# Kernel optimization log

Hardware: AMD Instinct MI355X
Metric: run time of the kernel (lower is better)

Reference implementation:

```python
import jax, jax.numpy as jnp
import numpy as np

DIM = 128
HEADS = 4
DIM_HEAD = 32
HIDDEN = HEADS * DIM_HEAD  # 128
SCALE = DIM_HEAD ** -0.5


def setup_inputs() -> dict:
    key = jax.random.key(0)
    k1, k2, k3, k4 = jax.random.split(key, 4)
    x = jax.random.normal(k1, (16, DIM, 128, 128), dtype=jnp.float32)
    # 1x1 convs are just channel matmuls: store as [out_ch, in_ch]
    w_qkv = jax.random.normal(k2, (3 * HIDDEN, DIM), dtype=jnp.float32) * (DIM ** -0.5)
    w_out = jax.random.normal(k3, (DIM, HIDDEN), dtype=jnp.float32) * (HIDDEN ** -0.5)
    b_out = jax.random.normal(k4, (DIM,), dtype=jnp.float32) * 0.01
    return {"x": x, "w_qkv": w_qkv, "w_out": w_out, "b_out": b_out}


def reference(x, w_qkv, w_out, b_out):
    b, c, h, w = x.shape
    n = h * w
    # 1x1 conv (no bias): [b, 3*hidden, h, w]
    qkv = jnp.einsum('bchw,oc->bohw', x, w_qkv)
    q, k, v = jnp.split(qkv, 3, axis=1)
    # b (heads d) h w -> b heads d n
    def to_heads(t):
        return t.reshape(b, HEADS, DIM_HEAD, n)
    q = to_heads(q) * SCALE
    k = jax.nn.softmax(to_heads(k), axis=-1)
    v = to_heads(v)
    # small d x e context per (b, head)
    context = jnp.einsum('bhdn,bhen->bhde', k, v)
    out = jnp.einsum('bhde,bhdn->bhen', context, q)  # [b, heads, e, n]
    out = out.reshape(b, HIDDEN, h, w)
    # 1x1 conv with bias
    return jnp.einsum('bchw,oc->bohw', out, w_out) + b_out[None, :, None, None]
```

## Files before the change

kernel.cpp:

```cpp
#include <hip/hip_runtime.h>

typedef float f4 __attribute__((ext_vector_type(4)));
typedef short s4 __attribute__((ext_vector_type(4)));
typedef short s8 __attribute__((ext_vector_type(8)));
typedef unsigned int u32;

#define SCALE 0.17677669529663687f

static __device__ __forceinline__ short bf16c(float f) {
  u32 u = __builtin_bit_cast(u32, f);
  u32 r = u + 0x7fffu + ((u >> 16) & 1u);
  return (short)(r >> 16);
}

static __device__ __forceinline__ f4 mfma32(s8 a, s8 b, f4 c) {
  return __builtin_amdgcn_mfma_f32_16x16x32_bf16(a, b, c, 0, 0, 0);
}
static __device__ __forceinline__ f4 bmm16(s4 a, s4 b, f4 c) {
  s8 A = {a[0], a[1], a[2], a[3], (short)0, (short)0, (short)0, (short)0};
  s8 B = {b[0], b[1], b[2], b[3], (short)0, (short)0, (short)0, (short)0};
  return __builtin_amdgcn_mfma_f32_16x16x32_bf16(A, B, c, 0, 0, 0);
}

#define XSTRIDE 280

__global__ __launch_bounds__(256) void ctx_kernel(
    const float* __restrict__ x, const float* __restrict__ wqkv,
    float* __restrict__ cp, float* __restrict__ zp)
{
  const int chunk = blockIdx.x, b = blockIdx.y;
  const int tid = threadIdx.x, lane = tid & 63, h = tid >> 6;
  __shared__ __align__(16) char lds[2 * 64 * XSTRIDE];

  s8 wf[4][4];
  {
    const int colr = lane & 15, g = lane >> 4;
#pragma unroll
    for (int s = 0; s < 4; ++s) {
      const int grow = (s < 2 ? 128 : 256) + h * 32 + (s & 1) * 16 + colr;
#pragma unroll
      for (int kc = 0; kc < 4; ++kc) {
        const float* src = wqkv + grow * 128 + kc * 32 + g * 8;
        const f4 a = *(const f4*)src;
        const f4 c2 = *(const f4*)(src + 4);
        s8 t = {bf16c(a[0]), bf16c(a[1]), bf16c(a[2]), bf16c(a[3]),
                bf16c(c2[0]), bf16c(c2[1]), bf16c(c2[2]), bf16c(c2[3])};
        wf[s][kc] = t;
      }
    }
  }

  f4 ctxacc[2][2];
#pragma unroll
  for (int a = 0; a < 2; ++a)
#pragma unroll
    for (int e2 = 0; e2 < 2; ++e2) ctxacc[a][e2] = (f4){0.f, 0.f, 0.f, 0.f};
  float zloc[2] = {0.f, 0.f};

  const float* xb = x + (size_t)b * 128 * 16384 + chunk * 1024;
  const int nq = tid & 15, ch = tid >> 4;
  f4 v[2][4];

  auto aload = [&](int tl) {
#pragma unroll
    for (int q = 0; q < 2; ++q) {
      const int c0 = ch * 4 + q * 64;
#pragma unroll
      for (int i = 0; i < 4; ++i)
        v[q][i] = *(const f4*)(xb + (size_t)(c0 + i) * 16384 + tl * 64 + nq * 4);
    }
  };
  auto awrite = [&](int buf) {
#pragma unroll
    for (int q = 0; q < 2; ++q) {
      const int c0 = ch * 4 + q * 64;
#pragma unroll
      for (int j = 0; j < 4; ++j) {
        s4 t = {bf16c(v[q][0][j]), bf16c(v[q][1][j]), bf16c(v[q][2][j]),
                bf16c(v[q][3][j])};
        *(s4*)(lds + buf * (64 * XSTRIDE) + (nq * 4 + j) * XSTRIDE + c0 * 2) = t;
      }
    }
  };
  auto compute = [&](int buf) {
#pragma unroll
    for (int nt = 0; nt < 4; ++nt) {
      const char* rp =
          lds + buf * (64 * XSTRIDE) + (nt * 16 + (lane & 15)) * XSTRIDE +
          (lane >> 4) * 16;
      s8 af[4];
#pragma unroll
      for (int kc = 0; kc < 4; ++kc) {
        const s4 lo = *(const s4*)(rp + kc * 64);
        const s4 hi = *(const s4*)(rp + kc * 64 + 8);
        af[kc] = __builtin_shufflevector(lo, hi, 0, 1, 2, 3, 4, 5, 6, 7);
      }
      f4 acc[4];
#pragma unroll
      for (int s = 0; s < 4; ++s) acc[s] = (f4){0.f, 0.f, 0.f, 0.f};
#pragma unroll
      for (int kc = 0; kc < 4; ++kc)
#pragma unroll
        for (int s = 0; s < 4; ++s)
          acc[s] = mfma32(af[kc], wf[s][kc], acc[s]);
      f4 e0, e1;
#pragma unroll
      for (int r = 0; r < 4; ++r) {
        e0[r] = __expf(acc[0][r]);
        e1[r] = __expf(acc[1][r]);
      }
      zloc[0] += e0[0] + e0[1] + e0[2] + e0[3];
      zloc[1] += e1[0] + e1[1] + e1[2] + e1[3];
      const s4 ea0 = {bf16c(e0[0]), bf16c(e0[1]), bf16c(e0[2]), bf16c(e0[3])};
      const s4 ea1 = {bf16c(e1[0]), bf16c(e1[1]), bf16c(e1[2]), bf16c(e1[3])};
      const s4 vb0 = {bf16c(acc[2][0]), bf16c(acc[2][1]), bf16c(acc[2][2]),
                      bf16c(acc[2][3])};
      const s4 vb1 = {bf16c(acc[3][0]), bf16c(acc[3][1]), bf16c(acc[3][2]),
                      bf16c(acc[3][3])};
      ctxacc[0][0] = bmm16(ea0, vb0, ctxacc[0][0]);
      ctxacc[0][1] = bmm16(ea0, vb1, ctxacc[0][1]);
      ctxacc[1][0] = bmm16(ea1, vb0, ctxacc[1][0]);
      ctxacc[1][1] = bmm16(ea1, vb1, ctxacc[1][1]);
    }
  };

  aload(0);
  awrite(0);
  __syncthreads();
  for (int tl = 0; tl < 16; ++tl) {
    if (tl < 15) aload(tl + 1);
    compute(tl & 1);
    if (tl < 15) awrite((tl + 1) & 1);
    __syncthreads();
  }

  {
    const size_t base = (size_t)((b * 4 + h) * 16 + chunk) * 1024;
    const int g4 = (lane >> 4) * 4, cc = lane & 15;
#pragma unroll
    for (int a = 0; a < 2; ++a)
#pragma unroll
      for (int e2 = 0; e2 < 2; ++e2)
#pragma unroll
        for (int r = 0; r < 4; ++r)
          cp[base + (size_t)(a * 16 + g4 + r) * 32 + e2 * 16 + cc] =
              ctxacc[a][e2][r];
  }
#pragma unroll
  for (int s = 0; s < 2; ++s) {
    float z = zloc[s];
    z += __shfl_xor(z, 16);
    z += __shfl_xor(z, 32);
    if (lane < 16)
      zp[((b * 4 + h) * 16 + chunk) * 32 + s * 16 + lane] = z;
  }
}

__global__ __launch_bounds__(256, 2) void makeP(
    const float* __restrict__ cp, const float* __restrict__ zp,
    const float* __restrict__ wout, const float* __restrict__ wqkv,
    unsigned short* __restrict__ Phi)
{
  const int rg = blockIdx.x, b = blockIdx.y, t = threadIdx.x;
  __shared__ float ctxn[4096];
  __shared__ float zs[128];
  __shared__ float Ms[16][129];

  if (t < 128) {
    float s = 0.f;
#pragma unroll
    for (int ch = 0; ch < 16; ++ch)
      s += zp[((size_t)(b * 4 + (t >> 5)) * 16 + ch) * 32 + (t & 31)];
    zs[t] = s;
  }
  __syncthreads();
  {
    const int i0 = t * 16;
    const int hh = i0 >> 10;
    f4 s0 = {0.f,0.f,0.f,0.f}, s1 = s0, s2 = s0, s3 = s0;
    const float* src = cp + ((size_t)(b * 4 + hh) * 16) * 1024 + (i0 & 1023);
#pragma unroll
    for (int ch = 0; ch < 16; ++ch) {
      const float* p = src + ch * 1024;
      s0 += *(const f4*)(p);
      s1 += *(const f4*)(p + 4);
      s2 += *(const f4*)(p + 8);
      s3 += *(const f4*)(p + 12);
    }
    const float zinv = 1.f / zs[i0 >> 5];
    *(f4*)(ctxn + i0)      = s0 * zinv;
    *(f4*)(ctxn + i0 + 4)  = s1 * zinv;
    *(f4*)(ctxn + i0 + 8)  = s2 * zinv;
    *(f4*)(ctxn + i0 + 12) = s3 * zinv;
  }
  __syncthreads();
  {
    const int o = t >> 4, hd0 = (t & 15) * 8;
    const int hh = hd0 >> 5;
    f4 wseg[8];
    const float* wp = wout + (size_t)(rg * 16 + o) * 128 + hh * 32;
#pragma unroll
    for (int i = 0; i < 8; ++i) wseg[i] = *(const f4*)(wp + i * 4);
#pragma unroll
    for (int j = 0; j < 8; ++j) {
      const float* cn = ctxn + (hd0 + j) * 32;
      f4 acc = {0.f, 0.f, 0.f, 0.f};
#pragma unroll
      for (int i = 0; i < 8; ++i) acc += wseg[i] * *(const f4*)(cn + i * 4);
      Ms[o][hd0 + j] = acc[0] + acc[1] + acc[2] + acc[3];
    }
  }
  __syncthreads();
  {
    const int o = t >> 4, c0 = (t & 15) * 8;
    f4 a0 = {0.f,0.f,0.f,0.f}, a1 = a0;
#pragma unroll 8
    for (int hd = 0; hd < 128; ++hd) {
      const float m = Ms[o][hd];
      const float* wp = wqkv + (size_t)hd * 128 + c0;
      a0 += m * *(const f4*)(wp);
      a1 += m * *(const f4*)(wp + 4);
    }
    a0 *= SCALE;
    a1 *= SCALE;
    s8 out = {bf16c(a0[0]), bf16c(a0[1]), bf16c(a0[2]), bf16c(a0[3]),
              bf16c(a1[0]), bf16c(a1[1]), bf16c(a1[2]), bf16c(a1[3])};
    *(s8*)(Phi + ((size_t)b * 128 + rg * 16 + o) * 128 + c0) = out;
  }
}

__global__ __launch_bounds__(256) void out_gemm(
    const float* __restrict__ x, const unsigned short* __restrict__ Phi,
    const float* __restrict__ bias, float* __restrict__ y)
{
  const int nb = blockIdx.x, b = blockIdx.y;
  const int tid = threadIdx.x, lane = tid & 63, w = tid >> 6;
  __shared__ __align__(16) char lds[128 * XSTRIDE];

  s8 pf[2][4];
#pragma unroll
  for (int ot2 = 0; ot2 < 2; ++ot2) {
    const int orow = (w * 2 + ot2) * 16 + (lane & 15);
#pragma unroll
    for (int kc = 0; kc < 4; ++kc)
      pf[ot2][kc] = *(const s8*)(Phi + ((size_t)b * 128 + orow) * 128 +
                                 kc * 32 + (lane >> 4) * 8);
  }

  const float* xb = x + (size_t)b * 128 * 16384 + (size_t)nb * 128;
  {
    const int nq = tid & 31, ch = tid >> 5;
#pragma unroll
    for (int q = 0; q < 4; ++q) {
      const int c0 = ch * 4 + q * 32;
      f4 v[4];
#pragma unroll
      for (int i = 0; i < 4; ++i)
        v[i] = *(const f4*)(xb + (size_t)(c0 + i) * 16384 + nq * 4);
#pragma unroll
      for (int j = 0; j < 4; ++j) {
        s4 t = {bf16c(v[0][j]), bf16c(v[1][j]), bf16c(v[2][j]), bf16c(v[3][j])};
        *(s4*)(lds + (nq * 4 + j) * XSTRIDE + c0 * 2) = t;
      }
    }
  }
  __syncthreads();

  f4 acc[8][2];
#pragma unroll
  for (int nt = 0; nt < 8; ++nt)
#pragma unroll
    for (int ot2 = 0; ot2 < 2; ++ot2) acc[nt][ot2] = (f4){0.f, 0.f, 0.f, 0.f};

#pragma unroll
  for (int nt = 0; nt < 8; ++nt) {
    const char* rp = lds + (nt * 16 + (lane & 15)) * XSTRIDE + (lane >> 4) * 16;
    s8 af[4];
#pragma unroll
    for (int kc = 0; kc < 4; ++kc) {
      const s4 lo = *(const s4*)(rp + kc * 64);
      const s4 hi = *(const s4*)(rp + kc * 64 + 8);
      af[kc] = __builtin_shufflevector(lo, hi, 0, 1, 2, 3, 4, 5, 6, 7);
    }
#pragma unroll
    for (int kc = 0; kc < 4; ++kc)
#pragma unroll
      for (int ot2 = 0; ot2 < 2; ++ot2)
        acc[nt][ot2] = mfma32(af[kc], pf[ot2][kc], acc[nt][ot2]);
  }

  const int g4 = (lane >> 4) * 4;
#pragma unroll
  for (int ot2 = 0; ot2 < 2; ++ot2) {
    const int o = (w * 2 + ot2) * 16 + (lane & 15);
    const float bv = bias[o];
    float* yo = y + ((size_t)b * 128 + o) * 16384 + (size_t)nb * 128;
#pragma unroll
    for (int nt = 0; nt < 8; ++nt) {
      f4 o4 = acc[nt][ot2];
      o4[0] += bv; o4[1] += bv; o4[2] += bv; o4[3] += bv;
      *(f4*)(yo + nt * 16 + g4) = o4;
    }
  }
}

extern "C" void kernel_launch(void* const* d_in, const int* in_sizes, int n_in,
                              void* d_out, int out_size, void* d_ws, size_t ws_size,
                              hipStream_t stream) {
  const float* x = (const float*)d_in[0];
  const float* wqkv = (const float*)d_in[1];
  const float* wout = (const float*)d_in[2];
  const float* bias = (const float*)d_in[3];
  float* cp = (float*)d_ws;
  float* zp = cp + 1048576;
  unsigned short* Phi = (unsigned short*)(cp + 1081344);
  float* y = (float*)d_out;

  ctx_kernel<<<dim3(16, 16), 256, 0, stream>>>(x, wqkv, cp, zp);
  makeP<<<dim3(8, 16), 256, 0, stream>>>(cp, zp, wout, wqkv, Phi);
  out_gemm<<<dim3(128, 16), 256, 0, stream>>>(x, Phi, bias, y);
}
```

Baseline: 108.1 us.

## Split context pass into more chunks and add separate partial-reduction kernel

Templatizes the context kernel on chunk count and launches it with 64 chunks per batch instead of 16, quadrupling the grid to raise occupancy and memory-level parallelism while streaming x. A new reduce_ctx kernel sums the larger set of partial context matrices and normalizers. A simplified makeP variant then consumes the pre-reduced values. This adds a launch and more partial-sum traffic through workspace, with a fallback to the old path when the workspace is too small.

Result: slower. 114.7 us (+6.2%).

```diff
diff --git a/kernel.cpp b/kernel.cpp
--- a/kernel.cpp
+++ b/kernel.cpp
@@ -24,10 +24,12 @@
 
 #define XSTRIDE 280
 
+template <int NCH>
 __global__ __launch_bounds__(256) void ctx_kernel(
     const float* __restrict__ x, const float* __restrict__ wqkv,
     float* __restrict__ cp, float* __restrict__ zp)
 {
+  constexpr int NT = 16384 / NCH / 64;
   const int chunk = blockIdx.x, b = blockIdx.y;
   const int tid = threadIdx.x, lane = tid & 63, h = tid >> 6;
   __shared__ __align__(16) char lds[2 * 64 * XSTRIDE];
@@ -57,7 +59,7 @@
     for (int e2 = 0; e2 < 2; ++e2) ctxacc[a][e2] = (f4){0.f, 0.f, 0.f, 0.f};
   float zloc[2] = {0.f, 0.f};
 
-  const float* xb = x + (size_t)b * 128 * 16384 + chunk * 1024;
+  const float* xb = x + (size_t)b * 128 * 16384 + chunk * (NT * 64);
   const int nq = tid & 15, ch = tid >> 4;
   f4 v[2][4];
 
@@ -127,15 +129,15 @@
   aload(0);
   awrite(0);
   __syncthreads();
-  for (int tl = 0; tl < 16; ++tl) {
-    if (tl < 15) aload(tl + 1);
+  for (int tl = 0; tl < NT; ++tl) {
+    if (tl < NT - 1) aload(tl + 1);
     compute(tl & 1);
-    if (tl < 15) awrite((tl + 1) & 1);
+    if (tl < NT - 1) awrite((tl + 1) & 1);
     __syncthreads();
   }
 
   {
-    const size_t base = (size_t)((b * 4 + h) * 16 + chunk) * 1024;
+    const size_t base = (size_t)((b * 4 + h) * NCH + chunk) * 1024;
     const int g4 = (lane >> 4) * 4, cc = lane & 15;
 #pragma unroll
     for (int a = 0; a < 2; ++a)
@@ -152,11 +154,88 @@
     z += __shfl_xor(z, 16);
     z += __shfl_xor(z, 32);
     if (lane < 16)
-      zp[((b * 4 + h) * 16 + chunk) * 32 + s * 16 + lane] = z;
-  }
-}
-
-__global__ __launch_bounds__(256, 2) void makeP(
+      zp[((b * 4 + h) * NCH + chunk) * 32 + s * 16 + lane] = z;
+  }
+}
+
+__global__ __launch_bounds__(256) void reduce_ctx(
+    const float* __restrict__ cp, const float* __restrict__ zp,
+    float* __restrict__ ctx_red, float* __restrict__ z_red)
+{
+  const int bh = blockIdx.x >> 2, part = blockIdx.x & 3;
+  const int t = threadIdx.x;
+  const int idx = part * 256 + t;
+  float s = 0.f;
+  const float* src = cp + (size_t)bh * 64 * 1024 + idx;
+#pragma unroll 8
+  for (int ch = 0; ch < 64; ++ch) s += src[ch * 1024];
+  ctx_red[(size_t)bh * 1024 + idx] = s;
+  if (part == 0 && t < 32) {
+    float z = 0.f;
+#pragma unroll 8
+    for (int ch = 0; ch < 64; ++ch) z += zp[((size_t)bh * 64 + ch) * 32 + t];
+    z_red[bh * 32 + t] = z;
+  }
+}
+
+__global__ __launch_bounds__(256, 2) void makeP_fast(
+    const float* __restrict__ ctx_red, const float* __restrict__ z_red,
+    const float* __restrict__ wout, const float* __restrict__ wqkv,
+    unsigned short* __restrict__ Phi)
+{
+  const int rg = blockIdx.x, b = blockIdx.y, t = threadIdx.x;
+  __shared__ float ctxn[4096];
+  __shared__ float zs[128];
+  __shared__ float Ms[16][129];
+
+  if (t < 128) zs[t] = z_red[(b * 4 + (t >> 5)) * 32 + (t & 31)];
+  __syncthreads();
+  {
+    const int i0 = t * 16, hh = i0 >> 10;
+    const float zinv = 1.f / zs[i0 >> 5];
+    const float* src = ctx_red + (size_t)(b * 4 + hh) * 1024 + (i0 & 1023);
+    *(f4*)(ctxn + i0)      = *(const f4*)(src)      * zinv;
+    *(f4*)(ctxn + i0 + 4)  = *(const f4*)(src + 4)  * zinv;
+    *(f4*)(ctxn + i0 + 8)  = *(const f4*)(src + 8)  * zinv;
+    *(f4*)(ctxn + i0 + 12) = *(const f4*)(src + 12) * zinv;
+  }
+  __syncthreads();
+  {
+    const int o = t >> 4, hd0 = (t & 15) * 8;
+    const int hh = hd0 >> 5;
+    f4 wseg[8];
+    const float* wp = wout + (size_t)(rg * 16 + o) * 128 + hh * 32;
+#pragma unroll
+    for (int i = 0; i < 8; ++i) wseg[i] = *(const f4*)(wp + i * 4);
+#pragma unroll
+    for (int j = 0; j < 8; ++j) {
+      const float* cn = ctxn + (hd0 + j) * 32;
+      f4 acc = {0.f, 0.f, 0.f, 0.f};
+#pragma unroll
+      for (int i = 0; i < 8; ++i) acc += wseg[i] * *(const f4*)(cn + i * 4);
+      Ms[o][hd0 + j] = acc[0] + acc[1] + acc[2] + acc[3];
+    }
+  }
+  __syncthreads();
+  {
+    const int o = t >> 4, c0 = (t & 15) * 8;
+    f4 a0 = {0.f,0.f,0.f,0.f}, a1 = a0;
+#pragma unroll 8
+    for (int hd = 0; hd < 128; ++hd) {
+      const float m = Ms[o][hd];
+      const float* wp = wqkv + (size_t)hd * 128 + c0;
+      a0 += m * *(const f4*)(wp);
+      a1 += m * *(const f4*)(wp + 4);
+    }
+    a0 *= SCALE;
+    a1 *= SCALE;
+    s8 out = {bf16c(a0[0]), bf16c(a0[1]), bf16c(a0[2]), bf16c(a0[3]),
+              bf16c(a1[0]), bf16c(a1[1]), bf16c(a1[2]), bf16c(a1[3])};
+    *(s8*)(Phi + ((size_t)b * 128 + rg * 16 + o) * 128 + c0) = out;
+  }
+}
+
+__global__ __launch_bounds__(256, 2) void makeP_full(
     const float* __restrict__ cp, const float* __restrict__ zp,
     const float* __restrict__ wout, const float* __restrict__ wqkv,
     unsigned short* __restrict__ Phi)
@@ -311,12 +390,29 @@
   const float* wqkv = (const float*)d_in[1];
   const float* wout = (const float*)d_in[2];
   const float* bias = (const float*)d_in[3];
-  float* cp = (float*)d_ws;
-  float* zp = cp + 1048576;
-  unsigned short* Phi = (unsigned short*)(cp + 1081344);
+  float* ws = (float*)d_ws;
   float* y = (float*)d_out;
 
-  ctx_kernel<<<dim3(16, 16), 256, 0, stream>>>(x, wqkv, cp, zp);
-  makeP<<<dim3(8, 16), 256, 0, stream>>>(cp, zp, wout, wqkv, Phi);
-  out_gemm<<<dim3(128, 16), 256, 0, stream>>>(x, Phi, bias, y);
-}
+  const size_t CPN64 = (size_t)16 * 4 * 64 * 1024;
+  const size_t ZPN64 = (size_t)16 * 4 * 64 * 32;
+  const size_t need64 = (CPN64 + ZPN64 + 65536 + 2048) * 4 + 262144 * 2;
+
+  if (ws_size >= need64) {
+    float* cp = ws;
+    float* zp = cp + CPN64;
+    float* ctx_red = zp + ZPN64;
+    float* z_red = ctx_red + 65536;
+    unsigned short* Phi = (unsigned short*)(z_red + 2048);
+    ctx_kernel<64><<<dim3(64, 16), 256, 0, stream>>>(x, wqkv, cp, zp);
+    reduce_ctx<<<dim3(256), 256, 0, stream>>>(cp, zp, ctx_red, z_red);
+    makeP_fast<<<dim3(8, 16), 256, 0, stream>>>(ctx_red, z_red, wout, wqkv, Phi);
+    out_gemm<<<dim3(128, 16), 256, 0, stream>>>(x, Phi, bias, y);
+  } else {
+    float* cp = ws;
+    float* zp = cp + 1048576;
+    unsigned short* Phi = (unsigned short*)(cp + 1081344);
+    ctx_kernel<16><<<dim3(16, 16), 256, 0, stream>>>(x, wqkv, cp, zp);
+    makeP_full<<<dim3(8, 16), 256, 0, stream>>>(cp, zp, wout, wqkv, Phi);
+    out_gemm<<<dim3(128, 16), 256, 0, stream>>>(x, Phi, bias, y);
+  }
+}
```

## Split ctx kernel per head and compute k·v context with full-K MFMA via LDS

Applied to the files above, without the earlier changes.

The context kernel now launches one block per (chunk, head, batch), so there are four times as many blocks, and each wave computes a single 16-row projection slice (k or v) instead of all four. The exp(k) and v tiles are staged in LDS transposed so the context MFMA can use the full 32-deep K, replacing the zero-padded half-empty MFMAs. The x tile is single-buffered and launch bounds request higher occupancy. In exchange, every head block reloads the same x tile from global memory (4x x reads), and each tile now needs an extra barrier.

New measurement: 120.5 us. 11.5% more time.

```diff
diff --git a/kernel.cpp b/kernel.cpp
--- a/kernel.cpp
+++ b/kernel.cpp
@@ -6,6 +6,8 @@
 typedef unsigned int u32;
 
 #define SCALE 0.17677669529663687f
+#define XSTRIDE 280
+#define TSTR 144
 
 static __device__ __forceinline__ short bf16c(float f) {
   u32 u = __builtin_bit_cast(u32, f);
@@ -16,50 +18,38 @@
 static __device__ __forceinline__ f4 mfma32(s8 a, s8 b, f4 c) {
   return __builtin_amdgcn_mfma_f32_16x16x32_bf16(a, b, c, 0, 0, 0);
 }
-static __device__ __forceinline__ f4 bmm16(s4 a, s4 b, f4 c) {
-  s8 A = {a[0], a[1], a[2], a[3], (short)0, (short)0, (short)0, (short)0};
-  s8 B = {b[0], b[1], b[2], b[3], (short)0, (short)0, (short)0, (short)0};
-  return __builtin_amdgcn_mfma_f32_16x16x32_bf16(A, B, c, 0, 0, 0);
-}
-
-#define XSTRIDE 280
-
-__global__ __launch_bounds__(256) void ctx_kernel(
+
+__global__ __launch_bounds__(256, 4) void ctx_kernel(
     const float* __restrict__ x, const float* __restrict__ wqkv,
     float* __restrict__ cp, float* __restrict__ zp)
 {
-  const int chunk = blockIdx.x, b = blockIdx.y;
-  const int tid = threadIdx.x, lane = tid & 63, h = tid >> 6;
-  __shared__ __align__(16) char lds[2 * 64 * XSTRIDE];
-
-  s8 wf[4][4];
-  {
-    const int colr = lane & 15, g = lane >> 4;
-#pragma unroll
-    for (int s = 0; s < 4; ++s) {
-      const int grow = (s < 2 ? 128 : 256) + h * 32 + (s & 1) * 16 + colr;
-#pragma unroll
-      for (int kc = 0; kc < 4; ++kc) {
-        const float* src = wqkv + grow * 128 + kc * 32 + g * 8;
-        const f4 a = *(const f4*)src;
-        const f4 c2 = *(const f4*)(src + 4);
-        s8 t = {bf16c(a[0]), bf16c(a[1]), bf16c(a[2]), bf16c(a[3]),
-                bf16c(c2[0]), bf16c(c2[1]), bf16c(c2[2]), bf16c(c2[3])};
-        wf[s][kc] = t;
-      }
-    }
-  }
-
-  f4 ctxacc[2][2];
-#pragma unroll
-  for (int a = 0; a < 2; ++a)
-#pragma unroll
-    for (int e2 = 0; e2 < 2; ++e2) ctxacc[a][e2] = (f4){0.f, 0.f, 0.f, 0.f};
-  float zloc[2] = {0.f, 0.f};
+  const int chunk = blockIdx.x, h = blockIdx.y, b = blockIdx.z;
+  const int tid = threadIdx.x, lane = tid & 63, w = tid >> 6;
+  __shared__ __align__(16) char xs[64 * XSTRIDE];
+  __shared__ __align__(16) char te[32 * TSTR];
+  __shared__ __align__(16) char tv[32 * TSTR];
+
+  s8 wf[4];
+  {
+    const int grow = (w < 2 ? 128 : 256) + h * 32 + (w & 1) * 16 + (lane & 15);
+    const int k0 = (lane >> 4) * 8;
+#pragma unroll
+    for (int kc = 0; kc < 4; ++kc) {
+      const float* src = wqkv + grow * 128 + kc * 32 + k0;
+      const f4 a = *(const f4*)src;
+      const f4 c2 = *(const f4*)(src + 4);
+      s8 t = {bf16c(a[0]), bf16c(a[1]), bf16c(a[2]), bf16c(a[3]),
+              bf16c(c2[0]), bf16c(c2[1]), bf16c(c2[2]), bf16c(c2[3])};
+      wf[kc] = t;
+    }
+  }
+
+  f4 ctxacc = {0.f, 0.f, 0.f, 0.f};
+  float zloc = 0.f;
 
   const float* xb = x + (size_t)b * 128 * 16384 + chunk * 1024;
   const int nq = tid & 15, ch = tid >> 4;
-  f4 v[2][4];
+  f4 ld[2][4];
 
   auto aload = [&](int tl) {
 #pragma unroll
@@ -67,27 +57,36 @@
       const int c0 = ch * 4 + q * 64;
 #pragma unroll
       for (int i = 0; i < 4; ++i)
-        v[q][i] = *(const f4*)(xb + (size_t)(c0 + i) * 16384 + tl * 64 + nq * 4);
+        ld[q][i] = *(const f4*)(xb + (size_t)(c0 + i) * 16384 + tl * 64 + nq * 4);
     }
   };
-  auto awrite = [&](int buf) {
+  auto awrite = [&]() {
 #pragma unroll
     for (int q = 0; q < 2; ++q) {
       const int c0 = ch * 4 + q * 64;
 #pragma unroll
       for (int j = 0; j < 4; ++j) {
-        s4 t = {bf16c(v[q][0][j]), bf16c(v[q][1][j]), bf16c(v[q][2][j]),
-                bf16c(v[q][3][j])};
-        *(s4*)(lds + buf * (64 * XSTRIDE) + (nq * 4 + j) * XSTRIDE + c0 * 2) = t;
+        s4 t = {bf16c(ld[q][0][j]), bf16c(ld[q][1][j]), bf16c(ld[q][2][j]),
+                bf16c(ld[q][3][j])};
+        *(s4*)(xs + (nq * 4 + j) * XSTRIDE + c0 * 2) = t;
       }
     }
   };
-  auto compute = [&](int buf) {
+
+  const int dh = w >> 1, eh = w & 1;
+  const char* ap = te + (dh * 16 + (lane & 15)) * TSTR + (lane >> 4) * 16;
+  const char* bp = tv + (eh * 16 + (lane & 15)) * TSTR + (lane >> 4) * 16;
+
+  aload(0);
+  awrite();
+  __syncthreads();
+
+  for (int tl = 0; tl < 16; ++tl) {
+    if (tl < 15) aload(tl + 1);
+
 #pragma unroll
     for (int nt = 0; nt < 4; ++nt) {
-      const char* rp =
-          lds + buf * (64 * XSTRIDE) + (nt * 16 + (lane & 15)) * XSTRIDE +
-          (lane >> 4) * 16;
+      const char* rp = xs + (nt * 16 + (lane & 15)) * XSTRIDE + (lane >> 4) * 16;
       s8 af[4];
 #pragma unroll
       for (int kc = 0; kc < 4; ++kc) {
@@ -95,42 +94,31 @@
         const s4 hi = *(const s4*)(rp + kc * 64 + 8);
         af[kc] = __builtin_shufflevector(lo, hi, 0, 1, 2, 3, 4, 5, 6, 7);
       }
-      f4 acc[4];
-#pragma unroll
-      for (int s = 0; s < 4; ++s) acc[s] = (f4){0.f, 0.f, 0.f, 0.f};
-#pragma unroll
-      for (int kc = 0; kc < 4; ++kc)
-#pragma unroll
-        for (int s = 0; s < 4; ++s)
-          acc[s] = mfma32(af[kc], wf[s][kc], acc[s]);
-      f4 e0, e1;
-#pragma unroll
-      for (int r = 0; r < 4; ++r) {
-        e0[r] = __expf(acc[0][r]);
-        e1[r] = __expf(acc[1][r]);
+      f4 acc = {0.f, 0.f, 0.f, 0.f};
+#pragma unroll
+      for (int kc = 0; kc < 4; ++kc) acc = mfma32(af[kc], wf[kc], acc);
+      const int wb = (lane & 15) * TSTR + (nt * 16 + (lane >> 4) * 4) * 2;
+      if (w < 2) {
+        f4 e;
+#pragma unroll
+        for (int r = 0; r < 4; ++r) e[r] = __expf(acc[r]);
+        zloc += e[0] + e[1] + e[2] + e[3];
+        s4 t = {bf16c(e[0]), bf16c(e[1]), bf16c(e[2]), bf16c(e[3])};
+        *(s4*)(te + w * 16 * TSTR + wb) = t;
+      } else {
+        s4 t = {bf16c(acc[0]), bf16c(acc[1]), bf16c(acc[2]), bf16c(acc[3])};
+        *(s4*)(tv + (w - 2) * 16 * TSTR + wb) = t;
       }
-      zloc[0] += e0[0] + e0[1] + e0[2] + e0[3];
-      zloc[1] += e1[0] + e1[1] + e1[2] + e1[3];
-      const s4 ea0 = {bf16c(e0[0]), bf16c(e0[1]), bf16c(e0[2]), bf16c(e0[3])};
-      const s4 ea1 = {bf16c(e1[0]), bf16c(e1[1]), bf16c(e1[2]), bf16c(e1[3])};
-      const s4 vb0 = {bf16c(acc[2][0]), bf16c(acc[2][1]), bf16c(acc[2][2]),
-                      bf16c(acc[2][3])};
-      const s4 vb1 = {bf16c(acc[3][0]), bf16c(acc[3][1]), bf16c(acc[3][2]),
-                      bf16c(acc[3][3])};
-      ctxacc[0][0] = bmm16(ea0, vb0, ctxacc[0][0]);
-      ctxacc[0][1] = bmm16(ea0, vb1, ctxacc[0][1]);
-      ctxacc[1][0] = bmm16(ea1, vb0, ctxacc[1][0]);
-      ctxacc[1][1] = bmm16(ea1, vb1, ctxacc[1][1]);
-    }
-  };
-
-  aload(0);
-  awrite(0);
-  __syncthreads();
-  for (int tl = 0; tl < 16; ++tl) {
-    if (tl < 15) aload(tl + 1);
-    compute(tl & 1);
-    if (tl < 15) awrite((tl + 1) & 1);
+    }
+    __syncthreads();
+
+#pragma unroll
+    for (int nk = 0; nk < 2; ++nk) {
+      const s8 a = *(const s8*)(ap + nk * 64);
+      const s8 v = *(const s8*)(bp + nk * 64);
+      ctxacc = mfma32(a, v, ctxacc);
+    }
+    if (tl < 15) awrite();
     __syncthreads();
   }
 
@@ -138,25 +126,19 @@
     const size_t base = (size_t)((b * 4 + h) * 16 + chunk) * 1024;
     const int g4 = (lane >> 4) * 4, cc = lane & 15;
 #pragma unroll
-    for (int a = 0; a < 2; ++a)
-#pragma unroll
-      for (int e2 = 0; e2 < 2; ++e2)
-#pragma unroll
-        for (int r = 0; r < 4; ++r)
-          cp[base + (size_t)(a * 16 + g4 + r) * 32 + e2 * 16 + cc] =
-              ctxacc[a][e2][r];
-  }
-#pragma unroll
-  for (int s = 0; s < 2; ++s) {
-    float z = zloc[s];
+    for (int r = 0; r < 4; ++r)
+      cp[base + (size_t)(dh * 16 + g4 + r) * 32 + eh * 16 + cc] = ctxacc[r];
+  }
+  if (w < 2) {
+    float z = zloc;
     z += __shfl_xor(z, 16);
     z += __shfl_xor(z, 32);
     if (lane < 16)
-      zp[((b * 4 + h) * 16 + chunk) * 32 + s * 16 + lane] = z;
-  }
-}
-
-__global__ __launch_bounds__(256, 2) void makeP(
+      zp[((b * 4 + h) * 16 + chunk) * 32 + w * 16 + lane] = z;
+  }
+}
+
+__global__ __launch_bounds__(256, 2) void makeP_full(
     const float* __restrict__ cp, const float* __restrict__ zp,
     const float* __restrict__ wout, const float* __restrict__ wqkv,
     unsigned short* __restrict__ Phi)
@@ -316,7 +298,7 @@
   unsigned short* Phi = (unsigned short*)(cp + 1081344);
   float* y = (float*)d_out;
 
-  ctx_kernel<<<dim3(16, 16), 256, 0, stream>>>(x, wqkv, cp, zp);
-  makeP<<<dim3(8, 16), 256, 0, stream>>>(cp, zp, wout, wqkv, Phi);
+  ctx_kernel<<<dim3(16, 4, 16), 256, 0, stream>>>(x, wqkv, cp, zp);
+  makeP_full<<<dim3(8, 16), 256, 0, stream>>>(cp, zp, wout, wqkv, Phi);
   out_gemm<<<dim3(128, 16), 256, 0, stream>>>(x, Phi, bias, y);
 }
```

## Pre-convert x to padded bf16 tiles and stream via global_load_lds with more chunks

Applied to the files above, without the earlier changes.

Adds a conversion kernel that writes x once as bf16 in a padded LDS-ready tile layout. The context and output kernels then copy those tiles straight into LDS with global_load_lds, replacing the per-use fp32 loads, bf16 conversion and transposed LDS stores. The context kernel is also split into 64 chunks per batch instead of 16 to raise parallelism. In exchange there is an extra kernel launch, an extra pass that writes and rereads a 35 MB bf16 copy of x, and a larger workspace; the old path remains as a fallback when the workspace is too small.

Result: slower. 164.2 us (+52.0%).

```diff
diff --git a/kernel.cpp b/kernel.cpp
--- a/kernel.cpp
+++ b/kernel.cpp
@@ -6,6 +6,9 @@
 typedef unsigned int u32;
 
 #define SCALE 0.17677669529663687f
+#define XROW 272
+#define IMGB 17408
+#define XSTRIDE 280
 
 static __device__ __forceinline__ short bf16c(float f) {
   u32 u = __builtin_bit_cast(u32, f);
@@ -22,15 +25,50 @@
   return __builtin_amdgcn_mfma_f32_16x16x32_bf16(A, B, c, 0, 0, 0);
 }
 
-#define XSTRIDE 280
-
-__global__ __launch_bounds__(256) void ctx_kernel(
-    const float* __restrict__ x, const float* __restrict__ wqkv,
+static __device__ __forceinline__ void gload_lds16(const void* g, void* l) {
+  __builtin_amdgcn_global_load_lds(
+      (const __attribute__((address_space(1))) void*)g,
+      (__attribute__((address_space(3))) void*)l, 16, 0, 0);
+}
+
+__global__ __launch_bounds__(512) void cvt16(
+    const float* __restrict__ x, char* __restrict__ x16)
+{
+  const int ng = blockIdx.x, b = blockIdx.y;
+  const int tid = threadIdx.x;
+  const int nq = tid & 15, ch = tid >> 4;
+  const int c0 = ch * 4;
+  const float* xb = x + (size_t)b * 128 * 16384 + ng * 256;
+  char* ib = x16 + ((size_t)(b * 256 + ng * 4)) * IMGB;
+
+  f4 ld[4][4];
+#pragma unroll
+  for (int im = 0; im < 4; ++im)
+#pragma unroll
+    for (int i = 0; i < 4; ++i)
+      ld[im][i] = *(const f4*)(xb + (size_t)(c0 + i) * 16384 + im * 64 + nq * 4);
+
+#pragma unroll
+  for (int im = 0; im < 4; ++im) {
+    char* imp = ib + im * IMGB;
+#pragma unroll
+    for (int j = 0; j < 4; ++j) {
+      s4 t = {bf16c(ld[im][0][j]), bf16c(ld[im][1][j]), bf16c(ld[im][2][j]),
+              bf16c(ld[im][3][j])};
+      *(s4*)(imp + (nq * 4 + j) * XROW + c0 * 2) = t;
+    }
+  }
+}
+
+template <int NCH>
+__global__ __launch_bounds__(256) void ctx_fast(
+    const char* __restrict__ x16, const float* __restrict__ wqkv,
     float* __restrict__ cp, float* __restrict__ zp)
 {
+  constexpr int TPT = 256 / NCH;
   const int chunk = blockIdx.x, b = blockIdx.y;
   const int tid = threadIdx.x, lane = tid & 63, h = tid >> 6;
-  __shared__ __align__(16) char lds[2 * 64 * XSTRIDE];
+  __shared__ __align__(16) char lds[2 * IMGB];
 
   s8 wf[4][4];
   {
@@ -57,52 +95,31 @@
     for (int e2 = 0; e2 < 2; ++e2) ctxacc[a][e2] = (f4){0.f, 0.f, 0.f, 0.f};
   float zloc[2] = {0.f, 0.f};
 
-  const float* xb = x + (size_t)b * 128 * 16384 + chunk * 1024;
-  const int nq = tid & 15, ch = tid >> 4;
-  f4 v[2][4];
-
-  auto aload = [&](int tl) {
-#pragma unroll
-    for (int q = 0; q < 2; ++q) {
-      const int c0 = ch * 4 + q * 64;
-#pragma unroll
-      for (int i = 0; i < 4; ++i)
-        v[q][i] = *(const f4*)(xb + (size_t)(c0 + i) * 16384 + tl * 64 + nq * 4);
-    }
+  const char* imgs = x16 + ((size_t)(b * 256 + chunk * TPT)) * IMGB;
+  const int w = h;
+
+  auto STAGE = [&](int t, int buf) {
+    const char* g = imgs + (size_t)t * IMGB;
+    char* l = lds + buf * IMGB;
+    for (int s = w; s < 17; s += 4)
+      gload_lds16(g + s * 1024 + (size_t)lane * 16, l + s * 1024);
   };
-  auto awrite = [&](int buf) {
-#pragma unroll
-    for (int q = 0; q < 2; ++q) {
-      const int c0 = ch * 4 + q * 64;
-#pragma unroll
-      for (int j = 0; j < 4; ++j) {
-        s4 t = {bf16c(v[q][0][j]), bf16c(v[q][1][j]), bf16c(v[q][2][j]),
-                bf16c(v[q][3][j])};
-        *(s4*)(lds + buf * (64 * XSTRIDE) + (nq * 4 + j) * XSTRIDE + c0 * 2) = t;
-      }
-    }
-  };
+
   auto compute = [&](int buf) {
 #pragma unroll
     for (int nt = 0; nt < 4; ++nt) {
       const char* rp =
-          lds + buf * (64 * XSTRIDE) + (nt * 16 + (lane & 15)) * XSTRIDE +
-          (lane >> 4) * 16;
+          lds + buf * IMGB + (nt * 16 + (lane & 15)) * XROW + (lane >> 4) * 16;
       s8 af[4];
 #pragma unroll
-      for (int kc = 0; kc < 4; ++kc) {
-        const s4 lo = *(const s4*)(rp + kc * 64);
-        const s4 hi = *(const s4*)(rp + kc * 64 + 8);
-        af[kc] = __builtin_shufflevector(lo, hi, 0, 1, 2, 3, 4, 5, 6, 7);
-      }
+      for (int kc = 0; kc < 4; ++kc) af[kc] = *(const s8*)(rp + kc * 64);
       f4 acc[4];
 #pragma unroll
       for (int s = 0; s < 4; ++s) acc[s] = (f4){0.f, 0.f, 0.f, 0.f};
 #pragma unroll
       for (int kc = 0; kc < 4; ++kc)
 #pragma unroll
-        for (int s = 0; s < 4; ++s)
-          acc[s] = mfma32(af[kc], wf[s][kc], acc[s]);
+        for (int s = 0; s < 4; ++s) acc[s] = mfma32(af[kc], wf[s][kc], acc[s]);
       f4 e0, e1;
 #pragma unroll
       for (int r = 0; r < 4; ++r) {
@@ -124,18 +141,16 @@
     }
   };
 
-  aload(0);
-  awrite(0);
-  __syncthreads();
-  for (int tl = 0; tl < 16; ++tl) {
-    if (tl < 15) aload(tl + 1);
-    compute(tl & 1);
-    if (tl < 15) awrite((tl + 1) & 1);
+  STAGE(0, 0);
+  __syncthreads();
+  for (int t = 0; t < TPT; ++t) {
+    if (t + 1 < TPT) STAGE(t + 1, (t + 1) & 1);
+    compute(t & 1);
     __syncthreads();
   }
 
   {
-    const size_t base = (size_t)((b * 4 + h) * 16 + chunk) * 1024;
+    const size_t base = (size_t)((b * 4 + h) * NCH + chunk) * 1024;
     const int g4 = (lane >> 4) * 4, cc = lane & 15;
 #pragma unroll
     for (int a = 0; a < 2; ++a)
@@ -152,11 +167,139 @@
     z += __shfl_xor(z, 16);
     z += __shfl_xor(z, 32);
     if (lane < 16)
-      zp[((b * 4 + h) * 16 + chunk) * 32 + s * 16 + lane] = z;
-  }
-}
-
-__global__ __launch_bounds__(256, 2) void makeP(
+      zp[((b * 4 + h) * NCH + chunk) * 32 + s * 16 + lane] = z;
+  }
+}
+
+template <int NCH>
+__global__ __launch_bounds__(256) void ctx_reg(
+    const float* __restrict__ x, const float* __restrict__ wqkv,
+    float* __restrict__ cp, float* __restrict__ zp)
+{
+  constexpr int NT = 16384 / NCH / 64;
+  const int chunk = blockIdx.x, b = blockIdx.y;
+  const int tid = threadIdx.x, lane = tid & 63, h = tid >> 6;
+  __shared__ __align__(16) char lds[2 * 64 * XSTRIDE];
+
+  s8 wf[4][4];
+  {
+    const int colr = lane & 15, g = lane >> 4;
+#pragma unroll
+    for (int s = 0; s < 4; ++s) {
+      const int grow = (s < 2 ? 128 : 256) + h * 32 + (s & 1) * 16 + colr;
+#pragma unroll
+      for (int kc = 0; kc < 4; ++kc) {
+        const float* src = wqkv + grow * 128 + kc * 32 + g * 8;
+        const f4 a = *(const f4*)src;
+        const f4 c2 = *(const f4*)(src + 4);
+        s8 t = {bf16c(a[0]), bf16c(a[1]), bf16c(a[2]), bf16c(a[3]),
+                bf16c(c2[0]), bf16c(c2[1]), bf16c(c2[2]), bf16c(c2[3])};
+        wf[s][kc] = t;
+      }
+    }
+  }
+  f4 ctxacc[2][2];
+#pragma unroll
+  for (int a = 0; a < 2; ++a)
+#pragma unroll
+    for (int e2 = 0; e2 < 2; ++e2) ctxacc[a][e2] = (f4){0.f, 0.f, 0.f, 0.f};
+  float zloc[2] = {0.f, 0.f};
+  const float* xb = x + (size_t)b * 128 * 16384 + chunk * (NT * 64);
+  const int nq = tid & 15, ch = tid >> 4;
+  f4 v[2][4];
+  auto aload = [&](int tl) {
+#pragma unroll
+    for (int q = 0; q < 2; ++q) {
+      const int c0 = ch * 4 + q * 64;
+#pragma unroll
+      for (int i = 0; i < 4; ++i)
+        v[q][i] = *(const f4*)(xb + (size_t)(c0 + i) * 16384 + tl * 64 + nq * 4);
+    }
+  };
+  auto awrite = [&](int buf) {
+#pragma unroll
+    for (int q = 0; q < 2; ++q) {
+      const int c0 = ch * 4 + q * 64;
+#pragma unroll
+      for (int j = 0; j < 4; ++j) {
+        s4 t = {bf16c(v[q][0][j]), bf16c(v[q][1][j]), bf16c(v[q][2][j]),
+                bf16c(v[q][3][j])};
+        *(s4*)(lds + buf * (64 * XSTRIDE) + (nq * 4 + j) * XSTRIDE + c0 * 2) = t;
+      }
+    }
+  };
+  auto compute = [&](int buf) {
+#pragma unroll
+    for (int nt = 0; nt < 4; ++nt) {
+      const char* rp = lds + buf * (64 * XSTRIDE) +
+                       (nt * 16 + (lane & 15)) * XSTRIDE + (lane >> 4) * 16;
+      s8 af[4];
+#pragma unroll
+      for (int kc = 0; kc < 4; ++kc) {
+        const s4 lo = *(const s4*)(rp + kc * 64);
+        const s4 hi = *(const s4*)(rp + kc * 64 + 8);
+        af[kc] = __builtin_shufflevector(lo, hi, 0, 1, 2, 3, 4, 5, 6, 7);
+      }
+      f4 acc[4];
+#pragma unroll
+      for (int s = 0; s < 4; ++s) acc[s] = (f4){0.f, 0.f, 0.f, 0.f};
+#pragma unroll
+      for (int kc = 0; kc < 4; ++kc)
+#pragma unroll
+        for (int s = 0; s < 4; ++s) acc[s] = mfma32(af[kc], wf[s][kc], acc[s]);
+      f4 e0, e1;
+#pragma unroll
+      for (int r = 0; r < 4; ++r) {
+        e0[r] = __expf(acc[0][r]);
+        e1[r] = __expf(acc[1][r]);
+      }
+      zloc[0] += e0[0] + e0[1] + e0[2] + e0[3];
+      zloc[1] += e1[0] + e1[1] + e1[2] + e1[3];
+      const s4 ea0 = {bf16c(e0[0]), bf16c(e0[1]), bf16c(e0[2]), bf16c(e0[3])};
+      const s4 ea1 = {bf16c(e1[0]), bf16c(e1[1]), bf16c(e1[2]), bf16c(e1[3])};
+      const s4 vb0 = {bf16c(acc[2][0]), bf16c(acc[2][1]), bf16c(acc[2][2]),
+                      bf16c(acc[2][3])};
+      const s4 vb1 = {bf16c(acc[3][0]), bf16c(acc[3][1]), bf16c(acc[3][2]),
+                      bf16c(acc[3][3])};
+      ctxacc[0][0] = bmm16(ea0, vb0, ctxacc[0][0]);
+      ctxacc[0][1] = bmm16(ea0, vb1, ctxacc[0][1]);
+      ctxacc[1][0] = bmm16(ea1, vb0, ctxacc[1][0]);
+      ctxacc[1][1] = bmm16(ea1, vb1, ctxacc[1][1]);
+    }
+  };
+  aload(0);
+  awrite(0);
+  __syncthreads();
+  for (int tl = 0; tl < NT; ++tl) {
+    if (tl < NT - 1) aload(tl + 1);
+    compute(tl & 1);
+    if (tl < NT - 1) awrite((tl + 1) & 1);
+    __syncthreads();
+  }
+  {
+    const size_t base = (size_t)((b * 4 + h) * NCH + chunk) * 1024;
+    const int g4 = (lane >> 4) * 4, cc = lane & 15;
+#pragma unroll
+    for (int a = 0; a < 2; ++a)
+#pragma unroll
+      for (int e2 = 0; e2 < 2; ++e2)
+#pragma unroll
+        for (int r = 0; r < 4; ++r)
+          cp[base + (size_t)(a * 16 + g4 + r) * 32 + e2 * 16 + cc] =
+              ctxacc[a][e2][r];
+  }
+#pragma unroll
+  for (int s = 0; s < 2; ++s) {
+    float z = zloc[s];
+    z += __shfl_xor(z, 16);
+    z += __shfl_xor(z, 32);
+    if (lane < 16)
+      zp[((b * 4 + h) * NCH + chunk) * 32 + s * 16 + lane] = z;
+  }
+}
+
+template <int NCH>
+__global__ __launch_bounds__(256, 2) void makeP_full(
     const float* __restrict__ cp, const float* __restrict__ zp,
     const float* __restrict__ wout, const float* __restrict__ wqkv,
     unsigned short* __restrict__ Phi)
@@ -168,19 +311,19 @@
 
   if (t < 128) {
     float s = 0.f;
-#pragma unroll
-    for (int ch = 0; ch < 16; ++ch)
-      s += zp[((size_t)(b * 4 + (t >> 5)) * 16 + ch) * 32 + (t & 31)];
+#pragma unroll 8
+    for (int ch = 0; ch < NCH; ++ch)
+      s += zp[((size_t)(b * 4 + (t >> 5)) * NCH + ch) * 32 + (t & 31)];
     zs[t] = s;
   }
   __syncthreads();
   {
     const int i0 = t * 16;
     const int hh = i0 >> 10;
-    f4 s0 = {0.f,0.f,0.f,0.f}, s1 = s0, s2 = s0, s3 = s0;
-    const float* src = cp + ((size_t)(b * 4 + hh) * 16) * 1024 + (i0 & 1023);
-#pragma unroll
-    for (int ch = 0; ch < 16; ++ch) {
+    f4 s0 = {0.f, 0.f, 0.f, 0.f}, s1 = s0, s2 = s0, s3 = s0;
+    const float* src = cp + ((size_t)(b * 4 + hh) * NCH) * 1024 + (i0 & 1023);
+#pragma unroll 8
+    for (int ch = 0; ch < NCH; ++ch) {
       const float* p = src + ch * 1024;
       s0 += *(const f4*)(p);
       s1 += *(const f4*)(p + 4);
@@ -188,9 +331,9 @@
       s3 += *(const f4*)(p + 12);
     }
     const float zinv = 1.f / zs[i0 >> 5];
-    *(f4*)(ctxn + i0)      = s0 * zinv;
-    *(f4*)(ctxn + i0 + 4)  = s1 * zinv;
-    *(f4*)(ctxn + i0 + 8)  = s2 * zinv;
+    *(f4*)(ctxn + i0) = s0 * zinv;
+    *(f4*)(ctxn + i0 + 4) = s1 * zinv;
+    *(f4*)(ctxn + i0 + 8) = s2 * zinv;
     *(f4*)(ctxn + i0 + 12) = s3 * zinv;
   }
   __syncthreads();
@@ -213,7 +356,7 @@
   __syncthreads();
   {
     const int o = t >> 4, c0 = (t & 15) * 8;
-    f4 a0 = {0.f,0.f,0.f,0.f}, a1 = a0;
+    f4 a0 = {0.f, 0.f, 0.f, 0.f}, a1 = a0;
 #pragma unroll 8
     for (int hd = 0; hd < 128; ++hd) {
       const float m = Ms[o][hd];
@@ -229,14 +372,71 @@
   }
 }
 
-__global__ __launch_bounds__(256) void out_gemm(
+__global__ __launch_bounds__(256) void out_fast(
+    const char* __restrict__ x16, const unsigned short* __restrict__ Phi,
+    const float* __restrict__ bias, float* __restrict__ y)
+{
+  const int nb = blockIdx.x, b = blockIdx.y;
+  const int tid = threadIdx.x, lane = tid & 63, w = tid >> 6;
+  __shared__ __align__(16) char lds[2 * IMGB];
+
+  s8 pf[2][4];
+#pragma unroll
+  for (int ot2 = 0; ot2 < 2; ++ot2) {
+    const int orow = (w * 2 + ot2) * 16 + (lane & 15);
+#pragma unroll
+    for (int kc = 0; kc < 4; ++kc)
+      pf[ot2][kc] = *(const s8*)(Phi + ((size_t)b * 128 + orow) * 128 +
+                                 kc * 32 + (lane >> 4) * 8);
+  }
+
+  const char* imgs = x16 + ((size_t)(b * 256 + nb * 2)) * IMGB;
+  for (int s = w; s < 34; s += 4)
+    gload_lds16(imgs + s * 1024 + (size_t)lane * 16, lds + s * 1024);
+  __syncthreads();
+
+  f4 acc[8][2];
+#pragma unroll
+  for (int nt = 0; nt < 8; ++nt)
+#pragma unroll
+    for (int ot2 = 0; ot2 < 2; ++ot2) acc[nt][ot2] = (f4){0.f, 0.f, 0.f, 0.f};
+
+#pragma unroll
+  for (int nt = 0; nt < 8; ++nt) {
+    const char* rp = lds + (nt >> 2) * IMGB +
+                     ((nt & 3) * 16 + (lane & 15)) * XROW + (lane >> 4) * 16;
+    s8 af[4];
+#pragma unroll
+    for (int kc = 0; kc < 4; ++kc) af[kc] = *(const s8*)(rp + kc * 64);
+#pragma unroll
+    for (int kc = 0; kc < 4; ++kc)
+#pragma unroll
+      for (int ot2 = 0; ot2 < 2; ++ot2)
+        acc[nt][ot2] = mfma32(af[kc], pf[ot2][kc], acc[nt][ot2]);
+  }
+
+  const int g4 = (lane >> 4) * 4;
+#pragma unroll
+  for (int ot2 = 0; ot2 < 2; ++ot2) {
+    const int o = (w * 2 + ot2) * 16 + (lane & 15);
+    const float bv = bias[o];
+    float* yo = y + ((size_t)b * 128 + o) * 16384 + (size_t)nb * 128;
+#pragma unroll
+    for (int nt = 0; nt < 8; ++nt) {
+      f4 o4 = acc[nt][ot2];
+      o4[0] += bv; o4[1] += bv; o4[2] += bv; o4[3] += bv;
+      *(f4*)(yo + nt * 16 + g4) = o4;
+    }
+  }
+}
+
+__global__ __launch_bounds__(256) void out_old(
     const float* __restrict__ x, const unsigned short* __restrict__ Phi,
     const float* __restrict__ bias, float* __restrict__ y)
 {
   const int nb = blockIdx.x, b = blockIdx.y;
   const int tid = threadIdx.x, lane = tid & 63, w = tid >> 6;
   __shared__ __align__(16) char lds[128 * XSTRIDE];
-
   s8 pf[2][4];
 #pragma unroll
   for (int ot2 = 0; ot2 < 2; ++ot2) {
@@ -246,7 +446,6 @@
       pf[ot2][kc] = *(const s8*)(Phi + ((size_t)b * 128 + orow) * 128 +
                                  kc * 32 + (lane >> 4) * 8);
   }
-
   const float* xb = x + (size_t)b * 128 * 16384 + (size_t)nb * 128;
   {
     const int nq = tid & 31, ch = tid >> 5;
@@ -265,13 +464,11 @@
     }
   }
   __syncthreads();
-
   f4 acc[8][2];
 #pragma unroll
   for (int nt = 0; nt < 8; ++nt)
 #pragma unroll
     for (int ot2 = 0; ot2 < 2; ++ot2) acc[nt][ot2] = (f4){0.f, 0.f, 0.f, 0.f};
-
 #pragma unroll
   for (int nt = 0; nt < 8; ++nt) {
     const char* rp = lds + (nt * 16 + (lane & 15)) * XSTRIDE + (lane >> 4) * 16;
@@ -288,7 +485,6 @@
       for (int ot2 = 0; ot2 < 2; ++ot2)
         acc[nt][ot2] = mfma32(af[kc], pf[ot2][kc], acc[nt][ot2]);
   }
-
   const int g4 = (lane >> 4) * 4;
 #pragma unroll
   for (int ot2 = 0; ot2 < 2; ++ot2) {
@@ -311,12 +507,28 @@
   const float* wqkv = (const float*)d_in[1];
   const float* wout = (const float*)d_in[2];
   const float* bias = (const float*)d_in[3];
-  float* cp = (float*)d_ws;
-  float* zp = cp + 1048576;
-  unsigned short* Phi = (unsigned short*)(cp + 1081344);
   float* y = (float*)d_out;
 
-  ctx_kernel<<<dim3(16, 16), 256, 0, stream>>>(x, wqkv, cp, zp);
-  makeP<<<dim3(8, 16), 256, 0, stream>>>(cp, zp, wout, wqkv, Phi);
-  out_gemm<<<dim3(128, 16), 256, 0, stream>>>(x, Phi, bias, y);
-}
+  const size_t X16_BYTES = (size_t)16 * 256 * IMGB;
+  const size_t CP64 = (size_t)16 * 4 * 64 * 1024;
+  const size_t ZP64 = (size_t)16 * 4 * 64 * 32;
+  const size_t need = X16_BYTES + (CP64 + ZP64) * 4 + 262144 * 2;
+
+  if (ws_size >= need) {
+    char* x16 = (char*)d_ws;
+    float* cp = (float*)(x16 + X16_BYTES);
+    float* zp = cp + CP64;
+    unsigned short* Phi = (unsigned short*)(zp + ZP64);
+    cvt16<<<dim3(64, 16), 512, 0, stream>>>(x, x16);
+    ctx_fast<64><<<dim3(64, 16), 256, 0, stream>>>(x16, wqkv, cp, zp);
+    makeP_full<64><<<dim3(8, 16), 256, 0, stream>>>(cp, zp, wout, wqkv, Phi);
+    out_fast<<<dim3(128, 16), 256, 0, stream>>>(x16, Phi, bias, y);
+  } else {
+    float* cp = (float*)d_ws;
+    float* zp = cp + 1048576;
+    unsigned short* Phi = (unsigned short*)(cp + 1081344);
+    ctx_reg<16><<<dim3(16, 16), 256, 0, stream>>>(x, wqkv, cp, zp);
+    makeP_full<16><<<dim3(8, 16), 256, 0, stream>>>(cp, zp, wout, wqkv, Phi);
+    out_old<<<dim3(128, 16), 256, 0, stream>>>(x, Phi, bias, y);
+  }
+}
```
